# Kernel tuning notes

Measured on AMD Instinct MI355X. Metric: run time of the kernel, lower is better.

## Reference

```python
import jax, jax.numpy as jnp
from jax import lax
import numpy as np

BN_EPS = 1e-5  # nn.BatchNorm2d default eps (eval mode with running stats)


def setup_inputs() -> dict:
    key = jax.random.key(0)
    ks = jax.random.split(key, 6)
    B, C, O, H, W = 4, 64, 64, 128, 128
    x = jax.random.normal(ks[0], (B, C, H, W), jnp.float32)
    # conv_offset: 27 = 3 * deform_groups * kh * kw output channels, zero-bias.
    # Scaled small to mimic the near-zero init of ModulatedDeformConv2dPack.
    w_off = jax.random.normal(ks[1], (27, C, 3, 3), jnp.float32) * 0.05
    b_off = jnp.zeros((27,), jnp.float32)
    weight = jax.random.normal(ks[2], (O, C, 3, 3), jnp.float32) * (1.0 / np.sqrt(C * 9))
    bias = jax.random.normal(ks[3], (O,), jnp.float32) * 0.1
    gamma = jax.random.normal(ks[4], (O,), jnp.float32) * 0.1 + 1.0
    beta = jax.random.normal(ks[5], (O,), jnp.float32) * 0.1
    running_mean = jnp.zeros((O,), jnp.float32)
    running_var = jnp.ones((O,), jnp.float32)
    return {"x": x, "w_off": w_off, "b_off": b_off, "weight": weight, "bias": bias,
            "gamma": gamma, "beta": beta, "running_mean": running_mean, "running_var": running_var}


def _dcn_bn_relu(x, w_off, b_off, weight, bias, gamma, beta, running_mean, running_var):
    B, C, H, W = x.shape
    O = weight.shape[0]
    K = 9  # 3x3 kernel taps
    # --- offset/mask conv (regular 3x3, stride 1, pad 1) ---
    off = lax.conv_general_dilated(x, w_off, (1, 1), ((1, 1), (1, 1)),
                                   dimension_numbers=("NCHW", "OIHW", "NCHW"))
    off = off + b_off[None, :, None, None]
    o1, o2, m = jnp.split(off, 3, axis=1)  # each [B,9,H,W]
    # mmcv layout: cat(o1,o2) then interpreted as (tap, [y,x]) pairs
    offset = jnp.concatenate([o1, o2], axis=1).reshape(B, K, 2, H, W)
    mask = jax.nn.sigmoid(m)  # [B,K,H,W]
    # --- sampling grid: p = (h - pad + i*dil + dy, w - pad + j*dil + dx) ---
    ky = (jnp.repeat(jnp.arange(3), 3) - 1).astype(x.dtype)  # [K]
    kx = (jnp.tile(jnp.arange(3), 3) - 1).astype(x.dtype)
    py = jnp.arange(H, dtype=x.dtype)[None, None, :, None] + ky[None, :, None, None] + offset[:, :, 0]
    px = jnp.arange(W, dtype=x.dtype)[None, None, None, :] + kx[None, :, None, None] + offset[:, :, 1]
    y0 = jnp.floor(py); x0 = jnp.floor(px)
    dy = py - y0; dx = px - x0  # [B,K,H,W]
    y0i = y0.astype(jnp.int32); x0i = x0.astype(jnp.int32)

    def gather(yi, xi):
        # zero outside bounds (mmcv bilinear semantics)
        valid = (yi >= 0) & (yi < H) & (xi >= 0) & (xi < W)
        yc = jnp.clip(yi, 0, H - 1)
        xc = jnp.clip(xi, 0, W - 1)
        g = jax.vmap(lambda xb, yb, xb2: xb[:, yb, xb2])(x, yc, xc)  # [B,C,K,H,W]
        return g * valid[:, None].astype(x.dtype)

    w00 = ((1 - dy) * (1 - dx))[:, None]
    w01 = ((1 - dy) * dx)[:, None]
    w10 = (dy * (1 - dx))[:, None]
    w11 = (dy * dx)[:, None]
    samp = (gather(y0i, x0i) * w00 + gather(y0i, x0i + 1) * w01 +
            gather(y0i + 1, x0i) * w10 + gather(y0i + 1, x0i + 1) * w11)
    samp = samp * mask[:, None]  # modulation, [B,C,K,H,W]
    # conv accumulation over (channel, tap)
    out = jnp.einsum("ock,bckhw->bohw", weight.reshape(O, C, K), samp)
    out = out + bias[None, :, None, None]
    # --- BatchNorm2d (eval, running stats) + ReLU ---
    scale = gamma / jnp.sqrt(running_var + BN_EPS)
    out = (out - running_mean[None, :, None, None]) * scale[None, :, None, None] + beta[None, :, None, None]
    return jax.nn.relu(out)


def reference(x, w_off, b_off, weight, bias, gamma, beta, running_mean, running_var):
    return _dcn_bn_relu(x, w_off, b_off, weight, bias, gamma, beta, running_mean, running_var)
```

## Files before the change

### kernel.cpp

```cpp
#include <hip/hip_runtime.h>
#include <hip/hip_bf16.h>


#define HH 128
#define WW 128
#define KP2 200

typedef __attribute__((ext_vector_type(8))) short bf16x8;
typedef __attribute__((ext_vector_type(4))) float f32x4;

__device__ __forceinline__ unsigned short f2bf(float f) {
    union { __hip_bfloat16 b; unsigned short u; } cv;
    cv.b = __float2bfloat16(f);
    return cv.u;
}
__device__ __forceinline__ float bf2f(unsigned short u) {
    union { unsigned int i; float f; } cv;
    cv.i = ((unsigned int)u) << 16;
    return cv.f;
}
__device__ __forceinline__ unsigned int cvt_pk_bf16(float a, float b) {
    unsigned int r;
    asm("v_cvt_pk_bf16_f32 %0, %1, %2" : "=v"(r) : "v"(a), "v"(b));
    return r;
}

#define WBM_ELEMS 36864
#define WBO_ELEMS 18432
#define XT_OFF    55296

__global__ __launch_bounds__(256) void transpose_kernel(
    const float* __restrict__ x,
    const float* __restrict__ w_off,
    const float* __restrict__ wgt,
    unsigned short* __restrict__ ws)
{
    __shared__ float tile[64 * 65];
    const int tid = threadIdx.x;

    {
        int t = blockIdx.x * 256 + tid;
        if (t < WBM_ELEMS) {
            int j = t & 7, lane = (t >> 3) & 63, nt = (t >> 9) & 3, kb = t >> 11;
            int k = kb * 32 + ((lane >> 4) << 3) + j;
            int n = nt * 16 + (lane & 15);
            int tap = k >> 6, c = k & 63;
            ws[t] = f2bf(wgt[n * 576 + c * 9 + tap]);
        } else if (t < WBM_ELEMS + WBO_ELEMS) {
            int t2 = t - WBM_ELEMS;
            int j = t2 & 7, lane = (t2 >> 3) & 63, nt = (t2 >> 9) & 1, kb = t2 >> 10;
            int k = kb * 32 + ((lane >> 4) << 3) + j;
            int n = nt * 16 + (lane & 15);
            int tap = k >> 6, c = k & 63;
            ws[t] = (n < 27) ? f2bf(w_off[n * 576 + c * 9 + tap]) : (unsigned short)0;
        }
    }

    const int bb  = blockIdx.x >> 8;
    const int hw0 = (blockIdx.x & 255) << 6;
    const float* xb = x + ((size_t)bb << 20);
#pragma unroll
    for (int it = 0; it < 16; ++it) {
        int idx = it * 256 + tid;
        int c = idx >> 6, i = idx & 63;
        tile[c * 65 + i] = xb[(c << 14) + hw0 + i];
    }
    __syncthreads();
    unsigned int* xtb = (unsigned int*)(ws + XT_OFF) + ((size_t)bb << 19);
#pragma unroll
    for (int it = 0; it < 8; ++it) {
        int idx = it * 256 + tid;
        int i = idx >> 5, c2 = idx & 31;
        xtb[(size_t)(hw0 + i) * 32 + c2] =
            cvt_pk_bf16(tile[(2 * c2) * 65 + i], tile[(2 * c2 + 1) * 65 + i]);
    }
}

__global__ __launch_bounds__(256) void DeformConv_14568529068723_kernel(
    const float* __restrict__ b_off,
    const float* __restrict__ bias,
    const float* __restrict__ gamma,
    const float* __restrict__ beta,
    const float* __restrict__ rmean,
    const float* __restrict__ rvar,
    const unsigned short* __restrict__ ws,
    float* __restrict__ out)
{
    __shared__ __align__(16) unsigned short samp[32 * KP2];
    __shared__ __align__(16) float eL[4][9][32];
    __shared__ int   oL[2][9][32];
    __shared__ float sbuf[176];

    const int tid  = threadIdx.x;
    const int wv   = tid >> 6;
    const int lane = tid & 63;
    const int px16 = lane & 15;
    const int cg   = lane >> 4;
    const int c8   = tid & 7;
    const int pxq  = tid >> 3;

    if (tid < 64) {
        float sc = gamma[tid] * __frsqrt_rn(rvar[tid] + 1e-5f);
        sbuf[tid] = sc;
        sbuf[64 + tid] = (bias[tid] - rmean[tid]) * sc + beta[tid];
        if (tid < 27) sbuf[128 + tid] = b_off[tid];
    }

    const int bid = blockIdx.x;
    const int swz = ((bid & 7) << 8) + (bid >> 3);
    const int p0   = swz * 32;
    const int b    = p0 >> 14;
    const int rem0 = p0 & 16383;
    const int h    = rem0 >> 7;
    const int w0   = rem0 & 127;
    const unsigned short* xt = ws + XT_OFF + ((size_t)b << 20);

    const bf16x8* WbM = (const bf16x8*)ws;
    const bf16x8* WbO = (const bf16x8*)(ws + WBM_ELEMS);

    unsigned short* rowbuf = (unsigned short*)eL;

    __syncthreads();

    f32x4 accO[2];
#pragma unroll
    for (int q = 0; q < 2; ++q) accO[q] = (f32x4){0.f, 0.f, 0.f, 0.f};

    for (int chk = 0; chk < 3; ++chk) {
        {
            int yy = h + chk - 1;
            int yc = min(max(yy, 0), HH - 1);
            bool oky = (yy >= 0) & (yy < HH);
            for (int i = tid; i < 272; i += 256) {
                int cc = i >> 3, c8i = i & 7;
                int gx = w0 - 1 + cc;
                bool ok = oky & (gx >= 0) & (gx < WW);
                int xc = min(max(gx, 0), WW - 1);
                uint4 v = *(const uint4*)(xt + (yc * WW + xc) * 64 + (c8i << 3));
                if (!ok) { v.x = 0u; v.y = 0u; v.z = 0u; v.w = 0u; }
                *(uint4*)&rowbuf[(cc * 64) + (((c8i ^ (cc & 7)) << 3))] = v;
            }
        }
        __syncthreads();
        if (wv < 2) {
            __builtin_amdgcn_s_setprio(1);
#pragma unroll
            for (int st = 0; st < 6; ++st) {
                int kb = chk * 6 + st;
                int tl = st >> 1;
                int g0 = (st & 1) * 4 + cg;
                bf16x8 bO = WbO[(kb * 2 + wv) * 64 + lane];
#pragma unroll
                for (int mt = 0; mt < 2; ++mt) {
                    int col = mt * 16 + px16 + tl;
                    bf16x8 af = *(const bf16x8*)&rowbuf[(col * 64) + (((g0 ^ (col & 7)) << 3))];
                    accO[mt] = __builtin_amdgcn_mfma_f32_16x16x32_bf16(af, bO, accO[mt], 0, 0, 0);
                }
            }
            __builtin_amdgcn_s_setprio(0);
        }
        __syncthreads();
    }
    float* offs = (float*)samp;
    if (wv < 2) {
        int n0 = wv * 16 + (lane & 15);
        int mB = cg * 4;
        if (n0 < 27) {
#pragma unroll
            for (int mt = 0; mt < 2; ++mt)
#pragma unroll
                for (int r = 0; r < 4; ++r) {
                    int pxc = mt * 16 + mB + r;
                    float vv = accO[mt][r] + sbuf[128 + n0];
                    if (n0 >= 18) vv = 1.0f / (1.0f + __expf(-vv));
                    offs[n0 * 32 + pxc] = vv;
                }
        }
    }
    __syncthreads();

#pragma unroll
    for (int base = 0; base < 288; base += 256) {
        int idx = base + tid;
        if (idx < 288) {
            int px = idx & 31, tap = idx >> 5;
            float o1 = offs[(2 * tap) * 32 + px];
            float o2 = offs[(2 * tap + 1) * 32 + px];
            float m  = offs[(18 + tap) * 32 + px];
            float py  = (float)(h + tap / 3 - 1) + o1;
            float pxf = (float)(w0 + px + tap % 3 - 1) + o2;
            float y0f = floorf(py), x0f = floorf(pxf);
            float dy = py - y0f, dx = pxf - x0f;
            int y0 = (int)y0f, x0 = (int)x0f;
            int y1 = y0 + 1, x1 = x0 + 1;
            int yc0 = min(max(y0, 0), HH - 1), yc1 = min(max(y1, 0), HH - 1);
            int xc0 = min(max(x0, 0), WW - 1), xc1 = min(max(x1, 0), WW - 1);
            float vy0 = (y0 >= 0 && y0 < HH) ? 1.0f : 0.0f;
            float vy1 = (y1 >= 0 && y1 < HH) ? 1.0f : 0.0f;
            float vx0 = (x0 >= 0 && x0 < WW) ? 1.0f : 0.0f;
            float vx1 = (x1 >= 0 && x1 < WW) ? 1.0f : 0.0f;
            float c00 = (1.0f - dy) * (1.0f - dx) * m * vy0 * vx0;
            float c01 = (1.0f - dy) * dx * m * vy0 * vx1;
            float c10 = dy * (1.0f - dx) * m * vy1 * vx0;
            float c11 = dy * dx * m * vy1 * vx1;
            int bx = min(xc0, WW - 2);
            bool s0 = (xc0 != bx), s1 = (xc1 != bx);
            eL[0][tap][px] = (s0 ? 0.f : c00) + (s1 ? 0.f : c01);
            eL[1][tap][px] = (s0 ? c00 : 0.f) + (s1 ? c01 : 0.f);
            eL[2][tap][px] = (s0 ? 0.f : c10) + (s1 ? 0.f : c11);
            eL[3][tap][px] = (s0 ? c10 : 0.f) + (s1 ? c11 : 0.f);
            oL[0][tap][px] = (yc0 * WW + bx) * 64;
            oL[1][tap][px] = (yc1 * WW + bx) * 64;
        }
    }
    __syncthreads();

    f32x4 acc[2];
#pragma unroll
    for (int mt = 0; mt < 2; ++mt) acc[mt] = (f32x4){0.f, 0.f, 0.f, 0.f};

    for (int chk = 0; chk < 3; ++chk) {
#pragma unroll
        for (int tl = 0; tl < 3; ++tl) {
            int tap = chk * 3 + tl;
            int o0 = oL[0][tap][pxq], o1r = oL[1][tap][pxq];
            float e0 = eL[0][tap][pxq], e1 = eL[1][tap][pxq];
            float e2 = eL[2][tap][pxq], e3 = eL[3][tap][pxq];
            uint4 a0 = *(const uint4*)(xt + o0 + (c8 << 3));
            uint4 a1 = *(const uint4*)(xt + o0 + 64 + (c8 << 3));
            uint4 b0 = *(const uint4*)(xt + o1r + (c8 << 3));
            uint4 b1 = *(const uint4*)(xt + o1r + 64 + (c8 << 3));
            const unsigned int* pa0 = (const unsigned int*)&a0;
            const unsigned int* pa1 = (const unsigned int*)&a1;
            const unsigned int* pb0 = (const unsigned int*)&b0;
            const unsigned int* pb1 = (const unsigned int*)&b1;
            uint4 pk;
            unsigned int* pp = (unsigned int*)&pk;
#pragma unroll
            for (int q = 0; q < 4; ++q) {
                float lo = e0 * bf2f((unsigned short)(pa0[q] & 0xffff))
                         + e1 * bf2f((unsigned short)(pa1[q] & 0xffff))
                         + e2 * bf2f((unsigned short)(pb0[q] & 0xffff))
                         + e3 * bf2f((unsigned short)(pb1[q] & 0xffff));
                float hi = e0 * bf2f((unsigned short)(pa0[q] >> 16))
                         + e1 * bf2f((unsigned short)(pa1[q] >> 16))
                         + e2 * bf2f((unsigned short)(pb0[q] >> 16))
                         + e3 * bf2f((unsigned short)(pb1[q] >> 16));
                pp[q] = cvt_pk_bf16(lo, hi);
            }
            *(uint4*)&samp[pxq * KP2 + tl * 64 + (c8 << 3)] = pk;
        }
        __syncthreads();
        __builtin_amdgcn_s_setprio(1);
#pragma unroll
        for (int st = 0; st < 6; ++st) {
            int kb = chk * 6 + st;
            bf16x8 bf = WbM[(kb * 4 + wv) * 64 + lane];
            bf16x8 af0 = *(const bf16x8*)&samp[px16 * KP2 + st * 32 + (cg << 3)];
            bf16x8 af1 = *(const bf16x8*)&samp[(16 + px16) * KP2 + st * 32 + (cg << 3)];
            acc[0] = __builtin_amdgcn_mfma_f32_16x16x32_bf16(af0, bf, acc[0], 0, 0, 0);
            acc[1] = __builtin_amdgcn_mfma_f32_16x16x32_bf16(af1, bf, acc[1], 0, 0, 0);
        }
        __builtin_amdgcn_s_setprio(0);
        __syncthreads();
    }

    float* dT = (float*)samp;
    {
        int n0 = lane & 15;
        int mB = cg * 4;
#pragma unroll
        for (int mt = 0; mt < 2; ++mt)
#pragma unroll
            for (int r = 0; r < 4; ++r)
                dT[(wv * 16 + n0) * 33 + mt * 16 + mB + r] = acc[mt][r];
    }
    __syncthreads();
    {
        int px = tid & 31;
        int oh = tid >> 5;
#pragma unroll
        for (int i = 0; i < 8; ++i) {
            int o = 8 * i + oh;
            float v = dT[o * 33 + px];
            v = fmaxf(fmaf(v, sbuf[o], sbuf[64 + o]), 0.0f);
            out[(((size_t)(b * 64 + o)) << 14) + rem0 + px] = v;
        }
    }
}

extern "C" void kernel_launch(void* const* d_in, const int* in_sizes, int n_in,
                              void* d_out, int out_size, void* d_ws, size_t ws_size,
                              hipStream_t stream) {
    (void)in_sizes; (void)n_in; (void)ws_size; (void)out_size;
    const float* x     = (const float*)d_in[0];
    const float* w_off = (const float*)d_in[1];
    const float* b_off = (const float*)d_in[2];
    const float* wgt   = (const float*)d_in[3];
    const float* bias  = (const float*)d_in[4];
    const float* gamma = (const float*)d_in[5];
    const float* beta  = (const float*)d_in[6];
    const float* rmean = (const float*)d_in[7];
    const float* rvar  = (const float*)d_in[8];
    unsigned short* wsB = (unsigned short*)d_ws;
    float* outp = (float*)d_out;

    transpose_kernel<<<dim3(1024), dim3(256), 0, stream>>>(x, w_off, wgt, wsB);
    DeformConv_14568529068723_kernel<<<dim3(2048), dim3(256), 0, stream>>>(
        b_off, bias, gamma, beta, rmean, rvar, wsB, outp);
}
```

Measured before the change: 111.7 us.

## Stage a 5-row input window in LDS and double-buffer per-tap sampling

Loads a 5x36 pixel window of the bf16 channels-last input into shared memory once per block. The offset conv and any bilinear samples that fall inside this window now read from LDS instead of global memory, with a global fallback flagged in the packed offset table. The sampling/MFMA loop is restructured per tap with a double-buffered sample tile, so the interpolation for the next tap overlaps the MFMAs of the current one. In exchange LDS use rises (about 23KB for the window), which may lower occupancy, and a data-dependent branch is added inside the interpolation.

```diff
diff --git a/kernel.cpp b/kernel.cpp
--- a/kernel.cpp
+++ b/kernel.cpp
@@ -4,7 +4,7 @@
 
 #define HH 128
 #define WW 128
-#define KP2 200
+#define KP2 72
 
 typedef __attribute__((ext_vector_type(8))) short bf16x8;
 typedef __attribute__((ext_vector_type(4))) float f32x4;
@@ -86,8 +86,9 @@
     const unsigned short* __restrict__ ws,
     float* __restrict__ out)
 {
-    __shared__ __align__(16) unsigned short samp[32 * KP2];
-    __shared__ __align__(16) float eL[4][9][32];
+    __shared__ __align__(16) unsigned short win[5 * 36 * 64];
+    __shared__ __align__(16) unsigned short samp2[2 * 32 * KP2];
+    __shared__ float eL[4][9][32];
     __shared__ int   oL[2][9][32];
     __shared__ float sbuf[176];
 
@@ -118,32 +119,26 @@
     const bf16x8* WbM = (const bf16x8*)ws;
     const bf16x8* WbO = (const bf16x8*)(ws + WBM_ELEMS);
 
-    unsigned short* rowbuf = (unsigned short*)eL;
-
+    for (int i = tid; i < 1440; i += 256) {
+        int j = i / 288, rem = i - j * 288;
+        int cc = rem >> 3, c8i = rem & 7;
+        int gr = h - 2 + j, gc = w0 - 2 + cc;
+        bool ok = (gr >= 0) & (gr < HH) & (gc >= 0) & (gc < WW);
+        int pos = min(max(gr, 0), HH - 1) * WW + min(max(gc, 0), WW - 1);
+        uint4 v = *(const uint4*)(xt + pos * 64 + (c8i << 3));
+        if (!ok) { v.x = 0u; v.y = 0u; v.z = 0u; v.w = 0u; }
+        *(uint4*)&win[(j * 36 + cc) * 64 + ((c8i ^ (cc & 7)) << 3)] = v;
+    }
     __syncthreads();
 
     f32x4 accO[2];
 #pragma unroll
     for (int q = 0; q < 2; ++q) accO[q] = (f32x4){0.f, 0.f, 0.f, 0.f};
 
-    for (int chk = 0; chk < 3; ++chk) {
-        {
-            int yy = h + chk - 1;
-            int yc = min(max(yy, 0), HH - 1);
-            bool oky = (yy >= 0) & (yy < HH);
-            for (int i = tid; i < 272; i += 256) {
-                int cc = i >> 3, c8i = i & 7;
-                int gx = w0 - 1 + cc;
-                bool ok = oky & (gx >= 0) & (gx < WW);
-                int xc = min(max(gx, 0), WW - 1);
-                uint4 v = *(const uint4*)(xt + (yc * WW + xc) * 64 + (c8i << 3));
-                if (!ok) { v.x = 0u; v.y = 0u; v.z = 0u; v.w = 0u; }
-                *(uint4*)&rowbuf[(cc * 64) + (((c8i ^ (cc & 7)) << 3))] = v;
-            }
-        }
-        __syncthreads();
-        if (wv < 2) {
-            __builtin_amdgcn_s_setprio(1);
+    if (wv < 2) {
+        __builtin_amdgcn_s_setprio(1);
+#pragma unroll
+        for (int chk = 0; chk < 3; ++chk) {
 #pragma unroll
             for (int st = 0; st < 6; ++st) {
                 int kb = chk * 6 + st;
@@ -152,16 +147,16 @@
                 bf16x8 bO = WbO[(kb * 2 + wv) * 64 + lane];
 #pragma unroll
                 for (int mt = 0; mt < 2; ++mt) {
-                    int col = mt * 16 + px16 + tl;
-                    bf16x8 af = *(const bf16x8*)&rowbuf[(col * 64) + (((g0 ^ (col & 7)) << 3))];
+                    int col = mt * 16 + px16 + tl + 1;
+                    bf16x8 af = *(const bf16x8*)&win[((chk + 1) * 36 + col) * 64
+                                                     + ((g0 ^ (col & 7)) << 3)];
                     accO[mt] = __builtin_amdgcn_mfma_f32_16x16x32_bf16(af, bO, accO[mt], 0, 0, 0);
                 }
             }
-            __builtin_amdgcn_s_setprio(0);
-        }
-        __syncthreads();
-    }
-    float* offs = (float*)samp;
+        }
+        __builtin_amdgcn_s_setprio(0);
+    }
+    float* offs = (float*)samp2;
     if (wv < 2) {
         int n0 = wv * 16 + (lane & 15);
         int mB = cg * 4;
@@ -209,7 +204,13 @@
             eL[1][tap][px] = (s0 ? c00 : 0.f) + (s1 ? c01 : 0.f);
             eL[2][tap][px] = (s0 ? 0.f : c10) + (s1 ? 0.f : c11);
             eL[3][tap][px] = (s0 ? c10 : 0.f) + (s1 ? c11 : 0.f);
-            oL[0][tap][px] = (yc0 * WW + bx) * 64;
+            int j0 = yc0 - (h - 2);
+            int j1 = yc1 - (h - 2);
+            int jc = bx - (w0 - 2);
+            bool inw = (j0 >= 0) & (j0 <= 4) & (j1 >= 0) & (j1 <= 4)
+                     & (jc >= 0) & (jc <= 34);
+            oL[0][tap][px] = inw ? ((int)0x80000000 | (j0 << 10) | (j1 << 6) | jc)
+                                 : ((yc0 * WW + bx) * 64);
             oL[1][tap][px] = (yc1 * WW + bx) * 64;
         }
     }
@@ -219,53 +220,67 @@
 #pragma unroll
     for (int mt = 0; mt < 2; ++mt) acc[mt] = (f32x4){0.f, 0.f, 0.f, 0.f};
 
-    for (int chk = 0; chk < 3; ++chk) {
-#pragma unroll
-        for (int tl = 0; tl < 3; ++tl) {
-            int tap = chk * 3 + tl;
-            int o0 = oL[0][tap][pxq], o1r = oL[1][tap][pxq];
-            float e0 = eL[0][tap][pxq], e1 = eL[1][tap][pxq];
-            float e2 = eL[2][tap][pxq], e3 = eL[3][tap][pxq];
-            uint4 a0 = *(const uint4*)(xt + o0 + (c8 << 3));
-            uint4 a1 = *(const uint4*)(xt + o0 + 64 + (c8 << 3));
-            uint4 b0 = *(const uint4*)(xt + o1r + (c8 << 3));
-            uint4 b1 = *(const uint4*)(xt + o1r + 64 + (c8 << 3));
-            const unsigned int* pa0 = (const unsigned int*)&a0;
-            const unsigned int* pa1 = (const unsigned int*)&a1;
-            const unsigned int* pb0 = (const unsigned int*)&b0;
-            const unsigned int* pb1 = (const unsigned int*)&b1;
-            uint4 pk;
-            unsigned int* pp = (unsigned int*)&pk;
-#pragma unroll
-            for (int q = 0; q < 4; ++q) {
-                float lo = e0 * bf2f((unsigned short)(pa0[q] & 0xffff))
-                         + e1 * bf2f((unsigned short)(pa1[q] & 0xffff))
-                         + e2 * bf2f((unsigned short)(pb0[q] & 0xffff))
-                         + e3 * bf2f((unsigned short)(pb1[q] & 0xffff));
-                float hi = e0 * bf2f((unsigned short)(pa0[q] >> 16))
-                         + e1 * bf2f((unsigned short)(pa1[q] >> 16))
-                         + e2 * bf2f((unsigned short)(pb0[q] >> 16))
-                         + e3 * bf2f((unsigned short)(pb1[q] >> 16));
-                pp[q] = cvt_pk_bf16(lo, hi);
-            }
-            *(uint4*)&samp[pxq * KP2 + tl * 64 + (c8 << 3)] = pk;
-        }
-        __syncthreads();
+    auto interp = [&](int tap) {
+        int p = oL[0][tap][pxq];
+        float e0 = eL[0][tap][pxq], e1 = eL[1][tap][pxq];
+        float e2 = eL[2][tap][pxq], e3 = eL[3][tap][pxq];
+        uint4 a0, a1, b0, b1;
+        if (p < 0) {
+            int jc = p & 63, j1 = (p >> 6) & 7, j0 = (p >> 10) & 7;
+            int sw0 = (c8 ^ (jc & 7)) << 3;
+            int sw1 = (c8 ^ ((jc + 1) & 7)) << 3;
+            a0 = *(const uint4*)&win[(j0 * 36 + jc    ) * 64 + sw0];
+            a1 = *(const uint4*)&win[(j0 * 36 + jc + 1) * 64 + sw1];
+            b0 = *(const uint4*)&win[(j1 * 36 + jc    ) * 64 + sw0];
+            b1 = *(const uint4*)&win[(j1 * 36 + jc + 1) * 64 + sw1];
+        } else {
+            int o1r = oL[1][tap][pxq];
+            a0 = *(const uint4*)(xt + p + (c8 << 3));
+            a1 = *(const uint4*)(xt + p + 64 + (c8 << 3));
+            b0 = *(const uint4*)(xt + o1r + (c8 << 3));
+            b1 = *(const uint4*)(xt + o1r + 64 + (c8 << 3));
+        }
+        const unsigned int* pa0 = (const unsigned int*)&a0;
+        const unsigned int* pa1 = (const unsigned int*)&a1;
+        const unsigned int* pb0 = (const unsigned int*)&b0;
+        const unsigned int* pb1 = (const unsigned int*)&b1;
+        uint4 pk;
+        unsigned int* pp = (unsigned int*)&pk;
+#pragma unroll
+        for (int q = 0; q < 4; ++q) {
+            float lo = e0 * bf2f((unsigned short)(pa0[q] & 0xffff))
+                     + e1 * bf2f((unsigned short)(pa1[q] & 0xffff))
+                     + e2 * bf2f((unsigned short)(pb0[q] & 0xffff))
+                     + e3 * bf2f((unsigned short)(pb1[q] & 0xffff));
+            float hi = e0 * bf2f((unsigned short)(pa0[q] >> 16))
+                     + e1 * bf2f((unsigned short)(pa1[q] >> 16))
+                     + e2 * bf2f((unsigned short)(pb0[q] >> 16))
+                     + e3 * bf2f((unsigned short)(pb1[q] >> 16));
+            pp[q] = cvt_pk_bf16(lo, hi);
+        }
+        *(uint4*)&samp2[(tap & 1) * (32 * KP2) + pxq * KP2 + (c8 << 3)] = pk;
+    };
+
+    interp(0);
+    __syncthreads();
+    for (int tap = 0; tap < 9; ++tap) {
         __builtin_amdgcn_s_setprio(1);
 #pragma unroll
-        for (int st = 0; st < 6; ++st) {
-            int kb = chk * 6 + st;
+        for (int st = 0; st < 2; ++st) {
+            int kb = tap * 2 + st;
             bf16x8 bf = WbM[(kb * 4 + wv) * 64 + lane];
-            bf16x8 af0 = *(const bf16x8*)&samp[px16 * KP2 + st * 32 + (cg << 3)];
-            bf16x8 af1 = *(const bf16x8*)&samp[(16 + px16) * KP2 + st * 32 + (cg << 3)];
+            const unsigned short* sb = &samp2[(tap & 1) * (32 * KP2) + st * 32 + (cg << 3)];
+            bf16x8 af0 = *(const bf16x8*)&sb[px16 * KP2];
+            bf16x8 af1 = *(const bf16x8*)&sb[(16 + px16) * KP2];
             acc[0] = __builtin_amdgcn_mfma_f32_16x16x32_bf16(af0, bf, acc[0], 0, 0, 0);
             acc[1] = __builtin_amdgcn_mfma_f32_16x16x32_bf16(af1, bf, acc[1], 0, 0, 0);
         }
         __builtin_amdgcn_s_setprio(0);
+        if (tap < 8) interp(tap + 1);
         __syncthreads();
     }
 
-    float* dT = (float*)samp;
+    float* dT = (float*)samp2;
     {
         int n0 = lane & 15;
         int mB = cg * 4;
```

Result: slower. 118.3 us (+6.0%).
